# Kernel optimization log

Hardware: AMD Instinct MI355X
Metric: run time of the kernel (lower is better)

## Reference

```python
import jax, jax.numpy as jnp
import numpy as np

B, N, DIM, HEADS, DH, EDGE, DEPTH, K = 4, 128, 256, 8, 64, 64, 2, 512
INNER = HEADS * DH
SCALE = DH ** -0.5


def _ln(x, g, b, eps=1e-5):
    m = x.mean(-1, keepdims=True)
    v = ((x - m) ** 2).mean(-1, keepdims=True)
    return (x - m) / jnp.sqrt(v + eps) * g + b


def _rotate_half(x):
    # interleaved pairs: (d r) with r=2 -> (-x2, x1)
    xp = x.reshape(x.shape[:-1] + (-1, 2))
    x1, x2 = xp[..., 0], xp[..., 1]
    return jnp.stack((-x2, x1), axis=-1).reshape(x.shape)


def _gated_res(x, res, gw):
    gate = jax.nn.sigmoid(jnp.concatenate((x, res, x - res), axis=-1) @ gw)
    return x * gate + res * (1 - gate)


def forward(nodes, edges, edge_ln_g, edge_ln_b, ln1_g, ln1_b, w_exp, b_exp,
            w_q, b_q, w_kv, b_kv, w_ekv, b_ekv, w_out, b_out, gate1_w,
            ln2_g, ln2_b, w_ff1, b_ff1, w_ff2, b_ff2, gate2_w, codebook):
    b, n = nodes.shape[:2]
    # LayerNorm edges over channel dim: (B,C,N,N) -> (B,N,N,C)
    e = _ln(jnp.transpose(edges, (0, 2, 3, 1)), edge_ln_g, edge_ln_b)
    # rotary frequencies over positions, repeated pairwise -> (1, N, DH)
    inv = 1.0 / (10000.0 ** (jnp.arange(0, DH, 2, dtype=jnp.float32) / DH))
    fr = jnp.repeat(jnp.arange(n, dtype=jnp.float32)[:, None] * inv[None, :], 2, axis=-1)
    cos, sin = jnp.cos(fr)[None], jnp.sin(fr)[None]

    def heads3(t):  # (B,N,H*D) -> (B*H,N,D)
        return t.reshape(b, n, HEADS, DH).transpose(0, 2, 1, 3).reshape(b * HEADS, n, DH)

    for i in range(DEPTH):
        # PreNorm + edge-conditioned attention
        x = _ln(nodes, ln1_g[i], ln1_b[i])
        x = x @ w_exp[i] + b_exp[i]
        q = x @ w_q[i] + b_q[i]
        k, v = jnp.split(x @ w_kv[i] + b_kv[i], 2, axis=-1)
        ekv = e @ w_ekv[i] + b_ekv[i]  # (B,N,N,INNER)
        q, k, v = heads3(q), heads3(k), heads3(v)
        ekv = ekv.reshape(b, n, n, HEADS, DH).transpose(0, 3, 1, 2, 4).reshape(b * HEADS, n, n, DH)
        q = q * cos + _rotate_half(q) * sin
        k = k * cos + _rotate_half(k) * sin
        kk = k[:, None, :, :] + ekv  # (BH, i, j, d)
        vv = v[:, None, :, :] + ekv
        sim = jnp.einsum('bid,bijd->bij', q, kk) * SCALE
        att = jax.nn.softmax(sim, axis=-1)
        out = jnp.einsum('bij,bijd->bid', att, vv)
        out = out.reshape(b, HEADS, n, DH).transpose(0, 2, 1, 3).reshape(b, n, INNER)
        out = out @ w_out[i] + b_out[i]
        nodes = _gated_res(out, nodes, gate1_w[i])
        # PreNorm + FeedForward
        h = _ln(nodes, ln2_g[i], ln2_b[i])
        h = jax.nn.gelu(h @ w_ff1[i] + b_ff1[i], approximate=False) @ w_ff2[i] + b_ff2[i]
        nodes = _gated_res(h, nodes, gate2_w[i])

    # VQ codebook nearest-neighbor lookup with straight-through estimator
    z = nodes.reshape(-1, DIM)
    d = (z * z).sum(-1, keepdims=True) - 2.0 * z @ codebook.T + (codebook * codebook).sum(-1)[None, :]
    idx = jnp.argmin(d, axis=-1)
    zq = codebook[idx].reshape(b, n, DIM)
    return nodes + jax.lax.stop_gradient(zq - nodes)


def setup_inputs() -> dict:
    key = jax.random.key(0)
    ks = jax.random.split(key, 16)
    s = 0.02
    inp = {
        'nodes': jax.random.normal(ks[0], (B, N, DIM), jnp.float32),
        'edges': jax.random.normal(ks[1], (B, EDGE, N, N), jnp.float32),
        'edge_ln_g': jnp.ones((EDGE,), jnp.float32),
        'edge_ln_b': jnp.zeros((EDGE,), jnp.float32),
        'ln1_g': jnp.ones((DEPTH, DIM), jnp.float32),
        'ln1_b': jnp.zeros((DEPTH, DIM), jnp.float32),
        'w_exp': s * jax.random.normal(ks[2], (DEPTH, DIM, INNER), jnp.float32),
        'b_exp': jnp.zeros((DEPTH, INNER), jnp.float32),
        'w_q': s * jax.random.normal(ks[3], (DEPTH, INNER, INNER), jnp.float32),
        'b_q': jnp.zeros((DEPTH, INNER), jnp.float32),
        'w_kv': s * jax.random.normal(ks[4], (DEPTH, INNER, 2 * INNER), jnp.float32),
        'b_kv': jnp.zeros((DEPTH, 2 * INNER), jnp.float32),
        'w_ekv': s * jax.random.normal(ks[5], (DEPTH, EDGE, INNER), jnp.float32),
        'b_ekv': jnp.zeros((DEPTH, INNER), jnp.float32),
        'w_out': s * jax.random.normal(ks[6], (DEPTH, INNER, DIM), jnp.float32),
        'b_out': jnp.zeros((DEPTH, DIM), jnp.float32),
        'gate1_w': s * jax.random.normal(ks[7], (DEPTH, 3 * DIM, 1), jnp.float32),
        'ln2_g': jnp.ones((DEPTH, DIM), jnp.float32),
        'ln2_b': jnp.zeros((DEPTH, DIM), jnp.float32),
        'w_ff1': s * jax.random.normal(ks[8], (DEPTH, DIM, 4 * DIM), jnp.float32),
        'b_ff1': jnp.zeros((DEPTH, 4 * DIM), jnp.float32),
        'w_ff2': s * jax.random.normal(ks[9], (DEPTH, 4 * DIM, DIM), jnp.float32),
        'b_ff2': jnp.zeros((DEPTH, DIM), jnp.float32),
        'gate2_w': s * jax.random.normal(ks[10], (DEPTH, 3 * DIM, 1), jnp.float32),
        'codebook': jax.random.uniform(ks[11], (K, DIM), jnp.float32, -1.0 / K, 1.0 / K),
    }
    return inp


def reference(nodes, edges, edge_ln_g, edge_ln_b, ln1_g, ln1_b, w_exp, b_exp,
              w_q, b_q, w_kv, b_kv, w_ekv, b_ekv, w_out, b_out, gate1_w,
              ln2_g, ln2_b, w_ff1, b_ff1, w_ff2, b_ff2, gate2_w, codebook):
    return forward(nodes, edges, edge_ln_g, edge_ln_b, ln1_g, ln1_b, w_exp, b_exp,
                   w_q, b_q, w_kv, b_kv, w_ekv, b_ekv, w_out, b_out, gate1_w,
                   ln2_g, ln2_b, w_ff1, b_ff1, w_ff2, b_ff2, gate2_w, codebook)
```

## Files before the change

kernel.cpp:

```cpp
#include <hip/hip_runtime.h>
#include <math.h>


#define DEV __device__ __forceinline__

constexpr int Bn = 4, Nn = 128, DIMn = 256, HEADSn = 8, DHn = 64, EDGEn = 64,
              DEPTHn = 2, Kn = 512, INNERn = 512;
constexpr int QKVW = 1536;
constexpr int PART = 131072;

DEV float wave_reduce_sum(float v) {
#pragma unroll
  for (int m = 32; m >= 1; m >>= 1) v += __shfl_xor(v, m);
  return v;
}

DEV float block_reduce_sum_256(float v, float* red) {
  v = wave_reduce_sum(v);
  int tid = threadIdx.x;
  if ((tid & 63) == 0) red[tid >> 6] = v;
  __syncthreads();
  v = red[0] + red[1] + red[2] + red[3];
  __syncthreads();
  return v;
}

DEV float gelu_exact(float x) {
  return 0.5f * x * (1.f + erff(x * 0.70710678118654752f));
}

__global__ __launch_bounds__(256) void prep_kernel(
    const float* __restrict__ edges, const float* __restrict__ eg,
    const float* __restrict__ eb, float* __restrict__ e,
    float* __restrict__ eT, float* __restrict__ cost, float* __restrict__ sint,
    const float* __restrict__ nodes_in, const float* __restrict__ ln1_g,
    const float* __restrict__ ln1_b, float* __restrict__ xln,
    float* __restrict__ nodes, const float* __restrict__ wek,
    const float* __restrict__ w_out, const float* __restrict__ bek,
    const float* __restrict__ b_out, float* __restrict__ W2,
    float* __restrict__ b_out2, const float* __restrict__ w_exp,
    const float* __restrict__ b_exp, const float* __restrict__ w_q,
    const float* __restrict__ b_q, const float* __restrict__ w_kv,
    const float* __restrict__ b_kv, float* __restrict__ WqkvF,
    float* __restrict__ bqkvF) {
  __shared__ __align__(16) float smem[4480];
  int blk = blockIdx.x;
  int tid = threadIdx.x;

  if (blk < 12) {
    int t = blk;
    int l = t / 6, seg = t % 6;
    int n = seg * 256 + tid;
    const float* W;
    int ldw;
    float acc;
    if (n < 512) {
      W = w_q + (size_t)l * 512 * 512 + n;
      ldw = 512;
      acc = b_q[l * 512 + n];
    } else {
      W = w_kv + (size_t)l * 512 * 1024 + (n - 512);
      ldw = 1024;
      acc = b_kv[l * 1024 + (n - 512)];
    }
    const float* be = b_exp + l * 512;
#pragma unroll 8
    for (int k = 0; k < 512; ++k) acc += be[k] * W[(size_t)k * ldw];
    bqkvF[l * 1536 + n] = acc;
  } else if (blk < 396) {
    int t = blk - 12;
    int l = t / 192, r = t % 192;
    int by = r / 24, bx = r % 24;
    float* As = smem;
    float* Bs = smem + 32 * 34;
    int n0 = bx * 64;
    const float* Aab = w_exp + (size_t)l * 256 * 512 + (size_t)(by * 32) * 512;
    const float* Wb;
    int ldw;
    if (n0 < 512) {
      Wb = w_q + (size_t)l * 512 * 512 + n0;
      ldw = 512;
    } else {
      Wb = w_kv + (size_t)l * 512 * 1024 + (n0 - 512);
      ldw = 1024;
    }
    int arow = tid >> 3, acol = (tid & 7) << 2;
    int brow = tid >> 4, bcol = (tid & 15) << 2;
    int tx = tid & 15, ty = tid >> 4;
    float4 a_nxt = *(const float4*)(Aab + (size_t)arow * 512 + acol);
    float4 b0_nxt = *(const float4*)(Wb + (size_t)brow * ldw + bcol);
    float4 b1_nxt = *(const float4*)(Wb + (size_t)(brow + 16) * ldw + bcol);
    float acc[2][4] = {};
    for (int k0 = 0; k0 < 512; k0 += 32) {
      As[(acol + 0) * 34 + arow] = a_nxt.x;
      As[(acol + 1) * 34 + arow] = a_nxt.y;
      As[(acol + 2) * 34 + arow] = a_nxt.z;
      As[(acol + 3) * 34 + arow] = a_nxt.w;
      *(float4*)&Bs[brow * 68 + bcol] = b0_nxt;
      *(float4*)&Bs[(brow + 16) * 68 + bcol] = b1_nxt;
      __syncthreads();
      int kn = k0 + 32;
      if (kn < 512) {
        a_nxt = *(const float4*)(Aab + (size_t)arow * 512 + kn + acol);
        b0_nxt = *(const float4*)(Wb + (size_t)(kn + brow) * ldw + bcol);
        b1_nxt = *(const float4*)(Wb + (size_t)(kn + brow + 16) * ldw + bcol);
      }
#pragma unroll
      for (int kk = 0; kk < 32; ++kk) {
        float2 av = *(const float2*)&As[kk * 34 + ty * 2];
        float4 bv = *(const float4*)&Bs[kk * 68 + tx * 4];
        acc[0][0] += av.x * bv.x;
        acc[0][1] += av.x * bv.y;
        acc[0][2] += av.x * bv.z;
        acc[0][3] += av.x * bv.w;
        acc[1][0] += av.y * bv.x;
        acc[1][1] += av.y * bv.y;
        acc[1][2] += av.y * bv.z;
        acc[1][3] += av.y * bv.w;
      }
      __syncthreads();
    }
#pragma unroll
    for (int u = 0; u < 2; ++u) {
      int d = by * 32 + ty * 2 + u;
      float4 o = {acc[u][0], acc[u][1], acc[u][2], acc[u][3]};
      *(float4*)(WqkvF + (size_t)l * 256 * 1536 + (size_t)d * 1536 + n0 +
                 tx * 4) = o;
    }
  } else if (blk < 908) {
    float* ets = smem;
    int eidx = blk - 396;
    int i = eidx & 127, b = eidx >> 7;
    int j = tid & 127;
    bool act = tid < 128;
    float vals[EDGEn];
    float m = 0.f, inv = 0.f;
    if (act) {
      const float* src = edges + (size_t)b * EDGEn * Nn * Nn + i * Nn + j;
      float s = 0.f;
#pragma unroll
      for (int c = 0; c < EDGEn; ++c) {
        float x = src[(size_t)c * (Nn * Nn)];
        vals[c] = x;
        s += x;
      }
      m = s * (1.0f / 64.0f);
      float s2 = 0.f;
#pragma unroll
      for (int c = 0; c < EDGEn; ++c) {
        float d = vals[c] - m;
        s2 += d * d;
      }
      inv = 1.f / sqrtf(s2 * (1.0f / 64.0f) + 1e-5f);
    }
    float* dst = e + ((size_t)(b * Nn + i) * EDGEn) * Nn + j;
    float* dstT = eT + ((size_t)(b * Nn + i) * Nn) * EDGEn;
#pragma unroll
    for (int ch = 0; ch < 2; ++ch) {
      if (act) {
#pragma unroll
        for (int cc = 0; cc < 32; ++cc) {
          int c = ch * 32 + cc;
          float o = (vals[c] - m) * inv * eg[c] + eb[c];
          dst[(size_t)c * Nn] = o;
          ets[j * 33 + cc] = o;
        }
      }
      __syncthreads();
      if (act) {
#pragma unroll
        for (int it = 0; it < 8; ++it) {
          int f4 = it * 128 + j;
          int jj = f4 >> 3, c4 = (f4 & 7) << 2;
          float4 o4 = {ets[jj * 33 + c4], ets[jj * 33 + c4 + 1],
                       ets[jj * 33 + c4 + 2], ets[jj * 33 + c4 + 3]};
          *(float4*)(dstT + (size_t)jj * EDGEn + ch * 32 + c4) = o4;
        }
      }
      __syncthreads();
    }
  } else if (blk < 972) {
    int t = blk - 908;
    int l = t >> 5, h = (t >> 2) & 7, nt = t & 3;
    float* As = smem;
    float* Bs = smem + 64 * 36;
    const float* wekl = wek + (size_t)l * 64 * 512 + h * 64;
    const float* woutl =
        w_out + (size_t)l * 512 * 256 + (size_t)(h * 64) * 256 + nt * 64;
    int tx = tid & 15, ty = tid >> 4;
    float acc[4][4] = {};
    for (int d0 = 0; d0 < 64; d0 += 32) {
      for (int f = tid; f < 512; f += 256) {
        int c = f >> 3, d4 = (f & 7) << 2;
        *(float4*)&As[c * 36 + d4] =
            *(const float4*)(wekl + (size_t)c * 512 + d0 + d4);
      }
      for (int f = tid; f < 512; f += 256) {
        int dd = f >> 4, n4 = (f & 15) << 2;
        *(float4*)&Bs[dd * 68 + n4] =
            *(const float4*)(woutl + (size_t)(d0 + dd) * 256 + n4);
      }
      __syncthreads();
#pragma unroll
      for (int dd = 0; dd < 32; ++dd) {
        float4 bv = *(const float4*)&Bs[dd * 68 + tx * 4];
#pragma unroll
        for (int u = 0; u < 4; ++u) {
          float a = As[(ty * 4 + u) * 36 + dd];
          acc[u][0] += a * bv.x;
          acc[u][1] += a * bv.y;
          acc[u][2] += a * bv.z;
          acc[u][3] += a * bv.w;
        }
      }
      __syncthreads();
    }
#pragma unroll
    for (int u = 0; u < 4; ++u) {
      float4 o = {acc[u][0], acc[u][1], acc[u][2], acc[u][3]};
      *(float4*)(W2 + (size_t)l * 512 * 256 +
                 (size_t)(h * 64 + ty * 4 + u) * 256 + nt * 64 + tx * 4) = o;
    }
  } else if (blk < 980) {
    int t = blk - 972;
    int l = t >> 2, nt = t & 3;
    float* part = smem;
    int nn = tid & 63, kq = tid >> 6;
    const float* wcol = w_out + (size_t)l * 512 * 256 + nt * 64 + nn;
    float acc = 0.f;
    for (int k = kq * 128; k < kq * 128 + 128; ++k)
      acc += bek[l * 512 + k] * wcol[(size_t)k * 256];
    part[tid] = acc;
    __syncthreads();
    if (tid < 64)
      b_out2[l * 256 + nt * 64 + nn] =
          b_out[l * 256 + nt * 64 + nn] + part[nn] + part[64 + nn] +
          part[128 + nn] + part[192 + nn];
  } else if (blk < 996) {
    int t = (blk - 980) * 256 + tid;
    if (t < Nn * 32) {
      int n = t >> 5, p = t & 31;
      float inv = powf(10000.f, -(float)(2 * p) / 64.f);
      float fr = (float)n * inv;
      cost[t] = cosf(fr);
      sint[t] = sinf(fr);
    }
  } else {
    float* red = smem;
    int row = blk - 996;
    float v = nodes_in[(size_t)row * DIMn + tid];
    nodes[(size_t)row * DIMn + tid] = v;
    float m = block_reduce_sum_256(v, red) * (1.0f / 256.0f);
    float d = v - m;
    float var = block_reduce_sum_256(d * d, red) * (1.0f / 256.0f);
    float inv = 1.f / sqrtf(var + 1e-5f);
    xln[(size_t)row * DIMn + tid] = d * inv * ln1_g[tid] + ln1_b[tid];
  }
}

__global__ __launch_bounds__(256) void gemm_kernel(
    const float* __restrict__ A, const float* __restrict__ A2, int aact,
    const float* __restrict__ W1, int N1, const float* __restrict__ b1,
    const float* __restrict__ W2n, int N2, const float* __restrict__ b2,
    const float* __restrict__ Wkb, int Ksplit, float* __restrict__ C, int M,
    int Ntot, int K, int kspan, int act, const float* __restrict__ cost,
    const float* __restrict__ sint, float* __restrict__ kT) {
  __shared__ float As[32][34];
  __shared__ __align__(16) float Bs[32][68];
  int tid = threadIdx.x;
  int bx = blockIdx.x, by = blockIdx.y, zid = blockIdx.z;
  int tx = tid & 15, ty = tid >> 4;
  int arow = tid >> 3, acol = (tid & 7) << 2;
  int brow = tid >> 4, bcol = (tid & 15) << 2;
  int col0 = bx * 64;
  const float* W = W1;
  const float* bias = b1;
  int Nw = N1, wcol = col0;
  if (W2n && col0 >= N1) {
    W = W2n;
    bias = b2;
    Nw = N2;
    wcol = col0 - N1;
  }
  int kb = zid * kspan, kend = kb + kspan;
  const float* arp = A + (size_t)(by * 32 + arow) * K;
  const float* arp2 = A2 ? A2 + (size_t)(by * 32 + arow) * K : nullptr;

  auto load_a = [&](int kpos) -> float4 {
    float4 a = *(const float4*)(arp + kpos + acol);
    if (arp2) {
      float4 a2 = *(const float4*)(arp2 + kpos + acol);
      a.x += a2.x;
      a.y += a2.y;
      a.z += a2.z;
      a.w += a2.w;
    }
    if (aact == 1) {
      a.x = gelu_exact(a.x);
      a.y = gelu_exact(a.y);
      a.z = gelu_exact(a.z);
      a.w = gelu_exact(a.w);
    }
    return a;
  };

  float4 a_nxt = load_a(kb);
  const float* w0p;
  const float* w1p;
  {
    int kr0 = kb + brow, kr1 = kb + brow + 16;
    w0p = (Ksplit && kr0 >= Ksplit)
              ? Wkb + (size_t)(kr0 - Ksplit) * Nw + wcol + bcol
              : W + (size_t)kr0 * Nw + wcol + bcol;
    w1p = (Ksplit && kr1 >= Ksplit)
              ? Wkb + (size_t)(kr1 - Ksplit) * Nw + wcol + bcol
              : W + (size_t)kr1 * Nw + wcol + bcol;
  }
  float4 b0_nxt = *(const float4*)w0p;
  float4 b1_nxt = *(const float4*)w1p;

  float acc[2][4] = {};
  for (int k0 = kb; k0 < kend; k0 += 32) {
    As[acol + 0][arow] = a_nxt.x;
    As[acol + 1][arow] = a_nxt.y;
    As[acol + 2][arow] = a_nxt.z;
    As[acol + 3][arow] = a_nxt.w;
    *(float4*)&Bs[brow][bcol] = b0_nxt;
    *(float4*)&Bs[brow + 16][bcol] = b1_nxt;
    __syncthreads();
    int kn = k0 + 32;
    if (kn < kend) {
      a_nxt = load_a(kn);
      int kr0 = kn + brow, kr1 = kn + brow + 16;
      w0p = (Ksplit && kr0 >= Ksplit)
                ? Wkb + (size_t)(kr0 - Ksplit) * Nw + wcol + bcol
                : W + (size_t)kr0 * Nw + wcol + bcol;
      w1p = (Ksplit && kr1 >= Ksplit)
                ? Wkb + (size_t)(kr1 - Ksplit) * Nw + wcol + bcol
                : W + (size_t)kr1 * Nw + wcol + bcol;
      b0_nxt = *(const float4*)w0p;
      b1_nxt = *(const float4*)w1p;
    }
#pragma unroll
    for (int kk = 0; kk < 32; ++kk) {
      float2 av = *(const float2*)&As[kk][ty * 2];
      float4 bv = *(const float4*)&Bs[kk][tx * 4];
      acc[0][0] += av.x * bv.x;
      acc[0][1] += av.x * bv.y;
      acc[0][2] += av.x * bv.z;
      acc[0][3] += av.x * bv.w;
      acc[1][0] += av.y * bv.x;
      acc[1][1] += av.y * bv.y;
      acc[1][2] += av.y * bv.z;
      acc[1][3] += av.y * bv.w;
    }
    __syncthreads();
  }
  int ccol = wcol + tx * 4;
  bool ksec = (act == 4) && (col0 >= 512) && (col0 < 1024);
  float* trans = (float*)Bs;
  float* Cz = C + (size_t)zid * M * Ntot;
#pragma unroll
  for (int u = 0; u < 2; ++u) {
    int r = by * 32 + ty * 2 + u;
    float o[4];
#pragma unroll
    for (int w = 0; w < 4; ++w)
      o[w] = acc[u][w] + (zid == 0 ? bias[ccol + w] : 0.f);
    if (act == 1) {
#pragma unroll
      for (int w = 0; w < 4; ++w) o[w] = gelu_exact(o[w]);
    } else if (act == 4 && col0 < 1024) {
      int n = r & 127;
      int p0 = (ccol & 63) >> 1;
      float c0 = cost[n * 32 + p0], s0 = sint[n * 32 + p0];
      float c1 = cost[n * 32 + p0 + 1], s1 = sint[n * 32 + p0 + 1];
      float x0 = o[0], x1 = o[1], x2 = o[2], x3 = o[3];
      o[0] = x0 * c0 - x1 * s0;
      o[1] = x1 * c0 + x0 * s0;
      o[2] = x2 * c1 - x3 * s1;
      o[3] = x3 * c1 + x2 * s1;
    }
    if (ksec) {
#pragma unroll
      for (int w = 0; w < 4; ++w) trans[(tx * 4 + w) * 33 + ty * 2 + u] = o[w];
    } else {
      float4 o4 = {o[0], o[1], o[2], o[3]};
      *(float4*)(Cz + (size_t)r * Ntot + col0 + tx * 4) = o4;
    }
  }
  if (ksec) {
    __syncthreads();
    int h = (col0 - 512) >> 6;
    int bb = (by * 32) >> 7;
#pragma unroll
    for (int q = 0; q < 2; ++q) {
      int f4 = tid * 2 + q;
      int dl = f4 >> 3, j4 = (f4 & 7) << 2;
      int jj = (by * 32 + j4) & 127;
      float4 o4 = {trans[dl * 33 + j4], trans[dl * 33 + j4 + 1],
                   trans[dl * 33 + j4 + 2], trans[dl * 33 + j4 + 3]};
      *(float4*)(kT + ((size_t)(bb * 8 + h) * 64 + dl) * 128 + jj) = o4;
    }
  }
}

__global__ __launch_bounds__(128) void attn_kernel(
    const float* __restrict__ qkv, const float* __restrict__ e,
    const float* __restrict__ eT, const float* __restrict__ kT,
    const float* __restrict__ wek, const float* __restrict__ w_out,
    const float* __restrict__ W2, float* __restrict__ proj) {
  __shared__ __align__(16) float qs[256];
  __shared__ __align__(16) float qes[256];
  __shared__ __align__(16) float att[512];
  __shared__ float avh[512];
  __shared__ float aeh[512];
  __shared__ float wekh[64 * 65];
  int blk = blockIdx.x;
  int iq = blk & 31;
  int bh = blk >> 5;
  int h = bh & 7, b = bh >> 3;
  int i0 = iq * 4;
  int row0 = b * 128 + i0;
  int tid = threadIdx.x;

  for (int f = tid; f < 256; f += 128) {
    int ii = f >> 6, d = f & 63;
    qs[f] = qkv[(size_t)(row0 + ii) * QKVW + h * 64 + d];
  }
  for (int f = tid; f < 4096; f += 128) {
    int c = f >> 6, d = f & 63;
    wekh[c * 65 + d] = wek[(size_t)c * INNERn + h * 64 + d];
  }
  __syncthreads();

  for (int f = tid; f < 256; f += 128) {
    int ii = f >> 6, c = f & 63;
    float acc = 0.f;
#pragma unroll
    for (int d = 0; d < 64; ++d) acc += qs[ii * 64 + d] * wekh[c * 65 + d];
    qes[f] = acc;
  }
  __syncthreads();

  int i2 = tid >> 5, j4 = tid & 31;
  float s0 = 0.f, s1 = 0.f, s2 = 0.f, s3 = 0.f;
  {
    const float* ktb = kT + ((size_t)bh * 64) * 128 + j4 * 4;
#pragma unroll
    for (int d4 = 0; d4 < 64; d4 += 4) {
      float4 q4 = *(const float4*)&qs[i2 * 64 + d4];
      float4 k0 = *(const float4*)(ktb + (size_t)(d4 + 0) * 128);
      float4 k1 = *(const float4*)(ktb + (size_t)(d4 + 1) * 128);
      float4 k2 = *(const float4*)(ktb + (size_t)(d4 + 2) * 128);
      float4 k3 = *(const float4*)(ktb + (size_t)(d4 + 3) * 128);
      s0 += q4.x * k0.x + q4.y * k1.x + q4.z * k2.x + q4.w * k3.x;
      s1 += q4.x * k0.y + q4.y * k1.y + q4.z * k2.y + q4.w * k3.y;
      s2 += q4.x * k0.z + q4.y * k1.z + q4.z * k2.z + q4.w * k3.z;
      s3 += q4.x * k0.w + q4.y * k1.w + q4.z * k2.w + q4.w * k3.w;
    }
    const float* eb = e + ((size_t)(row0 + i2) * 64) * 128 + j4 * 4;
#pragma unroll
    for (int c4 = 0; c4 < 64; c4 += 4) {
      float4 qe4 = *(const float4*)&qes[i2 * 64 + c4];
      float4 e0 = *(const float4*)(eb + (size_t)(c4 + 0) * 128);
      float4 e1 = *(const float4*)(eb + (size_t)(c4 + 1) * 128);
      float4 e2 = *(const float4*)(eb + (size_t)(c4 + 2) * 128);
      float4 e3 = *(const float4*)(eb + (size_t)(c4 + 3) * 128);
      s0 += qe4.x * e0.x + qe4.y * e1.x + qe4.z * e2.x + qe4.w * e3.x;
      s1 += qe4.x * e0.y + qe4.y * e1.y + qe4.z * e2.y + qe4.w * e3.y;
      s2 += qe4.x * e0.z + qe4.y * e1.z + qe4.z * e2.z + qe4.w * e3.z;
      s3 += qe4.x * e0.w + qe4.y * e1.w + qe4.z * e2.w + qe4.w * e3.w;
    }
    s0 *= 0.125f;
    s1 *= 0.125f;
    s2 *= 0.125f;
    s3 *= 0.125f;
  }
  {
    float mx = fmaxf(fmaxf(s0, s1), fmaxf(s2, s3));
#pragma unroll
    for (int m = 16; m >= 1; m >>= 1) mx = fmaxf(mx, __shfl_xor(mx, m));
    float p0 = expf(s0 - mx), p1 = expf(s1 - mx), p2 = expf(s2 - mx),
          p3 = expf(s3 - mx);
    float sm = p0 + p1 + p2 + p3;
#pragma unroll
    for (int m = 16; m >= 1; m >>= 1) sm += __shfl_xor(sm, m);
    float inv = 1.f / sm;
    float4 a4 = {p0 * inv, p1 * inv, p2 * inv, p3 * inv};
    *(float4*)&att[i2 * 128 + j4 * 4] = a4;
  }
  __syncthreads();

  {
    int d = tid & 63, half = tid >> 6;
    float av0 = 0.f, av1 = 0.f, av2 = 0.f, av3 = 0.f;
    float ae0 = 0.f, ae1 = 0.f, ae2 = 0.f, ae3 = 0.f;
    const float* vb = qkv + (size_t)(b * 128) * QKVW + 1024 + h * 64 + d;
    const float* etb = eT + ((size_t)row0 * 128) * 64 + d;
    for (int jq = 0; jq < 16; ++jq) {
      int jb = half * 64 + jq * 4;
      float4 a0 = *(const float4*)&att[0 * 128 + jb];
      float4 a1 = *(const float4*)&att[1 * 128 + jb];
      float4 a2 = *(const float4*)&att[2 * 128 + jb];
      float4 a3 = *(const float4*)&att[3 * 128 + jb];
#pragma unroll
      for (int t = 0; t < 4; ++t) {
        int j = jb + t;
        float vv = vb[(size_t)j * QKVW];
        float at0 = ((const float*)&a0)[t];
        float at1 = ((const float*)&a1)[t];
        float at2 = ((const float*)&a2)[t];
        float at3 = ((const float*)&a3)[t];
        av0 += at0 * vv;
        av1 += at1 * vv;
        av2 += at2 * vv;
        av3 += at3 * vv;
        float e0 = etb[(size_t)j * 64];
        float e1 = etb[8192 + (size_t)j * 64];
        float e2 = etb[16384 + (size_t)j * 64];
        float e3 = etb[24576 + (size_t)j * 64];
        ae0 += at0 * e0;
        ae1 += at1 * e1;
        ae2 += at2 * e2;
        ae3 += at3 * e3;
      }
    }
    avh[half * 256 + 0 * 64 + d] = av0;
    avh[half * 256 + 1 * 64 + d] = av1;
    avh[half * 256 + 2 * 64 + d] = av2;
    avh[half * 256 + 3 * 64 + d] = av3;
    aeh[half * 256 + 0 * 64 + d] = ae0;
    aeh[half * 256 + 1 * 64 + d] = ae1;
    aeh[half * 256 + 2 * 64 + d] = ae2;
    aeh[half * 256 + 3 * 64 + d] = ae3;
  }
  __syncthreads();

  for (int f = tid; f < 256; f += 128) {
    int ii = f >> 6, dd = f & 63;
    att[ii * 128 + dd] = avh[ii * 64 + dd] + avh[256 + ii * 64 + dd];
    att[ii * 128 + 64 + dd] = aeh[ii * 64 + dd] + aeh[256 + ii * 64 + dd];
  }
  __syncthreads();

  {
    int rp = tid >> 6, n4 = (tid & 63) << 2;
    int r0 = rp * 2, r1 = rp * 2 + 1;
    float o0[4] = {}, o1[4] = {};
    const float* wo = w_out + (size_t)(h * 64) * 256 + n4;
#pragma unroll 8
    for (int k = 0; k < 64; ++k) {
      float4 w4 = *(const float4*)(wo + (size_t)k * 256);
      float a0 = att[r0 * 128 + k];
      float a1 = att[r1 * 128 + k];
      o0[0] += a0 * w4.x;
      o0[1] += a0 * w4.y;
      o0[2] += a0 * w4.z;
      o0[3] += a0 * w4.w;
      o1[0] += a1 * w4.x;
      o1[1] += a1 * w4.y;
      o1[2] += a1 * w4.z;
      o1[3] += a1 * w4.w;
    }
    const float* w2 = W2 + (size_t)(h * 64) * 256 + n4;
#pragma unroll 8
    for (int k = 0; k < 64; ++k) {
      float4 w4 = *(const float4*)(w2 + (size_t)k * 256);
      float a0 = att[r0 * 128 + 64 + k];
      float a1 = att[r1 * 128 + 64 + k];
      o0[0] += a0 * w4.x;
      o0[1] += a0 * w4.y;
      o0[2] += a0 * w4.z;
      o0[3] += a0 * w4.w;
      o1[0] += a1 * w4.x;
      o1[1] += a1 * w4.y;
      o1[2] += a1 * w4.z;
      o1[3] += a1 * w4.w;
    }
    float* pp = proj + (size_t)h * PART;
    float4 v0 = {o0[0], o0[1], o0[2], o0[3]};
    float4 v1 = {o1[0], o1[1], o1[2], o1[3]};
    *(float4*)(pp + (size_t)(row0 + r0) * 256 + n4) = v0;
    *(float4*)(pp + (size_t)(row0 + r1) * 256 + n4) = v1;
  }
}

__global__ __launch_bounds__(256) void gate_ln_kernel(
    const float* __restrict__ x, int nparts, const float* __restrict__ badd,
    float* __restrict__ nodes, const float* __restrict__ gw,
    const float* __restrict__ lng, const float* __restrict__ lnb,
    float* __restrict__ xln) {
  __shared__ float red[4];
  int row = blockIdx.x, tid = threadIdx.x;
  size_t off = (size_t)row * DIMn + tid;
  float xv = x[off];
  for (int p = 1; p < nparts; ++p) xv += x[off + (size_t)p * PART];
  if (badd) xv += badd[tid];
  float rv = nodes[off];
  float pv =
      xv * gw[tid] + rv * gw[DIMn + tid] + (xv - rv) * gw[2 * DIMn + tid];
  float ssum = block_reduce_sum_256(pv, red);
  float gsig = 1.f / (1.f + expf(-ssum));
  float nv = xv * gsig + rv * (1.f - gsig);
  nodes[off] = nv;
  if (lng) {
    float m = block_reduce_sum_256(nv, red) * (1.0f / 256.0f);
    float d = nv - m;
    float var = block_reduce_sum_256(d * d, red) * (1.0f / 256.0f);
    float inv = 1.f / sqrtf(var + 1e-5f);
    xln[off] = d * inv * lng[tid] + lnb[tid];
  }
}

__global__ __launch_bounds__(256) void vq_kernel(
    const float* __restrict__ nodes, const float* __restrict__ codebook,
    float* __restrict__ out) {
  __shared__ __align__(16) float zs[4 * 256];
  __shared__ float wval[4][4];
  __shared__ int widx[4][4];
  __shared__ int fidx[4];
  int row0 = blockIdx.x * 4;
  int tid = threadIdx.x;
  for (int f = tid; f < 1024; f += 256) zs[f] = nodes[(size_t)row0 * DIMn + f];
  __syncthreads();
  int k1 = tid, k2 = tid + 256;
  const float4* c1p = (const float4*)(codebook + (size_t)k1 * DIMn);
  const float4* c2p = (const float4*)(codebook + (size_t)k2 * DIMn);
  float dot[4][2] = {};
  float cc0 = 0.f, cc1 = 0.f;
#pragma unroll 8
  for (int d4 = 0; d4 < 64; ++d4) {
    float4 c1 = c1p[d4], c2 = c2p[d4];
    cc0 += c1.x * c1.x + c1.y * c1.y + c1.z * c1.z + c1.w * c1.w;
    cc1 += c2.x * c2.x + c2.y * c2.y + c2.z * c2.z + c2.w * c2.w;
#pragma unroll
    for (int r = 0; r < 4; ++r) {
      float4 z = *(const float4*)&zs[r * 256 + d4 * 4];
      dot[r][0] += c1.x * z.x + c1.y * z.y + c1.z * z.z + c1.w * z.w;
      dot[r][1] += c2.x * z.x + c2.y * z.y + c2.z * z.z + c2.w * z.w;
    }
  }
  int lane = tid & 63, w = tid >> 6;
#pragma unroll
  for (int r = 0; r < 4; ++r) {
    float bv = cc0 - 2.f * dot[r][0];
    int bi = k1;
    float v2 = cc1 - 2.f * dot[r][1];
    if (v2 < bv) {
      bv = v2;
      bi = k2;
    }
#pragma unroll
    for (int m = 32; m >= 1; m >>= 1) {
      float ov = __shfl_xor(bv, m);
      int oi = __shfl_xor(bi, m);
      if (ov < bv || (ov == bv && oi < bi)) {
        bv = ov;
        bi = oi;
      }
    }
    if (lane == 0) {
      wval[r][w] = bv;
      widx[r][w] = bi;
    }
  }
  __syncthreads();
  if (tid < 4) {
    float bb = wval[tid][0];
    int bi = widx[tid][0];
    for (int t = 1; t < 4; ++t)
      if (wval[tid][t] < bb || (wval[tid][t] == bb && widx[tid][t] < bi)) {
        bb = wval[tid][t];
        bi = widx[tid][t];
      }
    fidx[tid] = bi;
  }
  __syncthreads();
  for (int f = tid; f < 1024; f += 256) {
    int r = f >> 8, d = f & 255;
    float zv = zs[f];
    float zq = codebook[(size_t)fidx[r] * DIMn + d];
    out[(size_t)(row0 + r) * DIMn + d] = zv + (zq - zv);
  }
}

extern "C" void kernel_launch(void* const* d_in, const int* in_sizes, int n_in,
                              void* d_out, int out_size, void* d_ws,
                              size_t ws_size, hipStream_t stream) {
  const float* nodes_in = (const float*)d_in[0];
  const float* edges = (const float*)d_in[1];
  const float* edge_ln_g = (const float*)d_in[2];
  const float* edge_ln_b = (const float*)d_in[3];
  const float* ln1_g = (const float*)d_in[4];
  const float* ln1_b = (const float*)d_in[5];
  const float* w_exp = (const float*)d_in[6];
  const float* b_exp = (const float*)d_in[7];
  const float* w_q = (const float*)d_in[8];
  const float* b_q = (const float*)d_in[9];
  const float* w_kv = (const float*)d_in[10];
  const float* b_kv = (const float*)d_in[11];
  const float* w_ekv = (const float*)d_in[12];
  const float* b_ekv = (const float*)d_in[13];
  const float* w_out = (const float*)d_in[14];
  const float* b_out = (const float*)d_in[15];
  const float* gate1_w = (const float*)d_in[16];
  const float* ln2_g = (const float*)d_in[17];
  const float* ln2_b = (const float*)d_in[18];
  const float* w_ff1 = (const float*)d_in[19];
  const float* b_ff1 = (const float*)d_in[20];
  const float* w_ff2 = (const float*)d_in[21];
  const float* b_ff2 = (const float*)d_in[22];
  const float* gate2_w = (const float*)d_in[23];
  const float* codebook = (const float*)d_in[24];

  float* ws = (float*)d_ws;
  float* e_buf = ws;
  float* eT_buf = e_buf + 4194304;
  float* cost = eT_buf + 4194304;
  float* sint = cost + 4096;
  float* nodes = sint + 4096;
  float* xln = nodes + 131072;
  float* qkvb = xln + 131072;
  float* kTb = qkvb + 786432;
  float* proj = kTb + 262144;
  float* ff1 = proj + 1048576;
  float* W2buf = ff1 + 1048576;
  float* bout2 = W2buf + 262144;
  float* WqkvF = bout2 + 512;
  float* bqkvF = WqkvF + 786432;

  prep_kernel<<<1508, 256, 0, stream>>>(
      edges, edge_ln_g, edge_ln_b, e_buf, eT_buf, cost, sint, nodes_in, ln1_g,
      ln1_b, xln, nodes, w_ekv, w_out, b_ekv, b_out, W2buf, bout2, w_exp,
      b_exp, w_q, b_q, w_kv, b_kv, WqkvF, bqkvF);

  for (int l = 0; l < DEPTHn; ++l) {
    gemm_kernel<<<dim3(24, 16, 1), 256, 0, stream>>>(
        xln, nullptr, 0, WqkvF + (size_t)l * 256 * 1536, 1536,
        bqkvF + l * 1536, nullptr, 0, nullptr, nullptr, 0, qkvb, 512, QKVW,
        256, 256, 4, cost, sint, kTb);
    attn_kernel<<<1024, 128, 0, stream>>>(qkvb, e_buf, eT_buf, kTb,
                                          w_ekv + l * 64 * 512,
                                          w_out + l * 512 * 256,
                                          W2buf + l * 512 * 256, proj);
    gate_ln_kernel<<<512, 256, 0, stream>>>(
        proj, 8, bout2 + l * 256, nodes, gate1_w + l * 768, ln2_g + l * 256,
        ln2_b + l * 256, xln);
    gemm_kernel<<<dim3(16, 16, 2), 256, 0, stream>>>(
        xln, nullptr, 0, w_ff1 + l * 256 * 1024, 1024, b_ff1 + l * 1024,
        nullptr, 0, nullptr, nullptr, 0, ff1, 512, 1024, 256, 128, 0, cost,
        sint, nullptr);
    gemm_kernel<<<dim3(4, 16, 4), 256, 0, stream>>>(
        ff1, ff1 + 524288, 1, w_ff2 + l * 1024 * 256, 256, b_ff2 + l * 256,
        nullptr, 0, nullptr, nullptr, 0, proj, 512, 256, 1024, 256, 0, cost,
        sint, nullptr);
    const float* nlng = (l + 1 < DEPTHn) ? ln1_g + (l + 1) * 256 : nullptr;
    const float* nlnb = (l + 1 < DEPTHn) ? ln1_b + (l + 1) * 256 : nullptr;
    gate_ln_kernel<<<512, 256, 0, stream>>>(proj, 4, nullptr, nodes,
                                            gate2_w + l * 768, nlng, nlnb,
                                            xln);
  }
  vq_kernel<<<128, 256, 0, stream>>>(nodes, codebook, (float*)d_out);
}
```

Baseline: 319.0 us.

## Move edge LayerNorm and weight folding into first QKV gemm launch

After: 331.8 us. 1.04x slower.

```diff
diff --git a/kernel.cpp b/kernel.cpp
--- a/kernel.cpp
+++ b/kernel.cpp
@@ -29,21 +29,140 @@
   return 0.5f * x * (1.f + erff(x * 0.70710678118654752f));
 }
 
+
+DEV void edge_ln_block(int eidx, const float* __restrict__ edges,
+                       const float* __restrict__ eg,
+                       const float* __restrict__ eb, float* __restrict__ e,
+                       float* __restrict__ eT, float* smem) {
+  float* ets = smem;
+  float* redS = smem + 4224;
+  float* redQ = smem + 4480;
+  int tid = threadIdx.x;
+  int i = eidx & 127, b = eidx >> 7;
+  int j = tid & 127, half = tid >> 7;
+  const float* src = edges + (size_t)b * EDGEn * Nn * Nn +
+                     (size_t)(half * 32) * (Nn * Nn) + i * Nn + j;
+  float vals[32];
+  float s = 0.f, q = 0.f;
+#pragma unroll
+  for (int cc = 0; cc < 32; ++cc) {
+    float x = src[(size_t)cc * (Nn * Nn)];
+    vals[cc] = x;
+    s += x;
+    q += x * x;
+  }
+  redS[tid] = s;
+  redQ[tid] = q;
+  __syncthreads();
+  float ts = redS[j] + redS[j + 128];
+  float tq = redQ[j] + redQ[j + 128];
+  float m = ts * (1.0f / 64.0f);
+  float var = tq * (1.0f / 64.0f) - m * m;
+  float inv = 1.f / sqrtf(var + 1e-5f);
+  float* dst = e + ((size_t)(b * Nn + i) * EDGEn) * Nn + j;
+#pragma unroll
+  for (int cc = 0; cc < 32; ++cc) {
+    int c = half * 32 + cc;
+    float o = (vals[cc] - m) * inv * eg[c] + eb[c];
+    vals[cc] = o;
+    dst[(size_t)c * Nn] = o;
+  }
+  float* dstT = eT + ((size_t)(b * Nn + i) * Nn) * EDGEn;
+#pragma unroll
+  for (int ch = 0; ch < 2; ++ch) {
+    __syncthreads();
+    if (half == ch) {
+#pragma unroll
+      for (int cc = 0; cc < 32; ++cc) ets[j * 33 + cc] = vals[cc];
+    }
+    __syncthreads();
+#pragma unroll
+    for (int it = 0; it < 4; ++it) {
+      int f4 = it * 256 + tid;
+      int jj = f4 >> 3, c4 = (f4 & 7) << 2;
+      float4 o4 = {ets[jj * 33 + c4], ets[jj * 33 + c4 + 1],
+                   ets[jj * 33 + c4 + 2], ets[jj * 33 + c4 + 3]};
+      *(float4*)(dstT + (size_t)jj * EDGEn + ch * 32 + c4) = o4;
+    }
+  }
+}
+
+DEV void w2_fold_block(int t, const float* __restrict__ wek,
+                       const float* __restrict__ w_out, float* __restrict__ W2,
+                       float* smem) {
+  int l = t >> 5, h = (t >> 2) & 7, nt = t & 3;
+  float* As = smem;
+  float* Bs = smem + 2304;
+  const float* wekl = wek + (size_t)l * 64 * 512 + h * 64;
+  const float* woutl =
+      w_out + (size_t)l * 512 * 256 + (size_t)(h * 64) * 256 + nt * 64;
+  int tid = threadIdx.x;
+  int tx = tid & 15, ty = tid >> 4;
+  float acc[4][4] = {};
+  for (int d0 = 0; d0 < 64; d0 += 32) {
+    for (int f = tid; f < 512; f += 256) {
+      int c = f >> 3, d4 = (f & 7) << 2;
+      *(float4*)&As[c * 36 + d4] =
+          *(const float4*)(wekl + (size_t)c * 512 + d0 + d4);
+    }
+    for (int f = tid; f < 512; f += 256) {
+      int dd = f >> 4, n4 = (f & 15) << 2;
+      *(float4*)&Bs[dd * 68 + n4] =
+          *(const float4*)(woutl + (size_t)(d0 + dd) * 256 + n4);
+    }
+    __syncthreads();
+#pragma unroll
+    for (int dd = 0; dd < 32; ++dd) {
+      float4 bv = *(const float4*)&Bs[dd * 68 + tx * 4];
+#pragma unroll
+      for (int u = 0; u < 4; ++u) {
+        float a = As[(ty * 4 + u) * 36 + dd];
+        acc[u][0] += a * bv.x;
+        acc[u][1] += a * bv.y;
+        acc[u][2] += a * bv.z;
+        acc[u][3] += a * bv.w;
+      }
+    }
+    __syncthreads();
+  }
+#pragma unroll
+  for (int u = 0; u < 4; ++u) {
+    float4 o = {acc[u][0], acc[u][1], acc[u][2], acc[u][3]};
+    *(float4*)(W2 + (size_t)l * 512 * 256 + (size_t)(h * 64 + ty * 4 + u) * 256 +
+               nt * 64 + tx * 4) = o;
+  }
+}
+
+DEV void bout2_block(int t, const float* __restrict__ w_out,
+                     const float* __restrict__ bek,
+                     const float* __restrict__ b_out,
+                     float* __restrict__ b_out2, float* smem) {
+  int l = t >> 2, nt = t & 3;
+  float* part = smem;
+  int tid = threadIdx.x;
+  int nn = tid & 63, kq = tid >> 6;
+  const float* wcol = w_out + (size_t)l * 512 * 256 + nt * 64 + nn;
+  float acc = 0.f;
+  for (int k = kq * 128; k < kq * 128 + 128; ++k)
+    acc += bek[l * 512 + k] * wcol[(size_t)k * 256];
+  part[tid] = acc;
+  __syncthreads();
+  if (tid < 64)
+    b_out2[l * 256 + nt * 64 + nn] =
+        b_out[l * 256 + nt * 64 + nn] + part[nn] + part[64 + nn] +
+        part[128 + nn] + part[192 + nn];
+}
+
 __global__ __launch_bounds__(256) void prep_kernel(
-    const float* __restrict__ edges, const float* __restrict__ eg,
-    const float* __restrict__ eb, float* __restrict__ e,
-    float* __restrict__ eT, float* __restrict__ cost, float* __restrict__ sint,
-    const float* __restrict__ nodes_in, const float* __restrict__ ln1_g,
-    const float* __restrict__ ln1_b, float* __restrict__ xln,
-    float* __restrict__ nodes, const float* __restrict__ wek,
-    const float* __restrict__ w_out, const float* __restrict__ bek,
-    const float* __restrict__ b_out, float* __restrict__ W2,
-    float* __restrict__ b_out2, const float* __restrict__ w_exp,
-    const float* __restrict__ b_exp, const float* __restrict__ w_q,
-    const float* __restrict__ b_q, const float* __restrict__ w_kv,
-    const float* __restrict__ b_kv, float* __restrict__ WqkvF,
-    float* __restrict__ bqkvF) {
-  __shared__ __align__(16) float smem[4480];
+    const float* __restrict__ cost_dummy, float* __restrict__ cost,
+    float* __restrict__ sint, const float* __restrict__ nodes_in,
+    const float* __restrict__ ln1_g, const float* __restrict__ ln1_b,
+    float* __restrict__ xln, float* __restrict__ nodes,
+    const float* __restrict__ w_exp, const float* __restrict__ b_exp,
+    const float* __restrict__ w_q, const float* __restrict__ b_q,
+    const float* __restrict__ w_kv, const float* __restrict__ b_kv,
+    float* __restrict__ WqkvF, float* __restrict__ bqkvF) {
+  __shared__ __align__(16) float smem[3264];
   int blk = blockIdx.x;
   int tid = threadIdx.x;
 
@@ -127,117 +246,8 @@
       *(float4*)(WqkvF + (size_t)l * 256 * 1536 + (size_t)d * 1536 + n0 +
                  tx * 4) = o;
     }
-  } else if (blk < 908) {
-    float* ets = smem;
-    int eidx = blk - 396;
-    int i = eidx & 127, b = eidx >> 7;
-    int j = tid & 127;
-    bool act = tid < 128;
-    float vals[EDGEn];
-    float m = 0.f, inv = 0.f;
-    if (act) {
-      const float* src = edges + (size_t)b * EDGEn * Nn * Nn + i * Nn + j;
-      float s = 0.f;
-#pragma unroll
-      for (int c = 0; c < EDGEn; ++c) {
-        float x = src[(size_t)c * (Nn * Nn)];
-        vals[c] = x;
-        s += x;
-      }
-      m = s * (1.0f / 64.0f);
-      float s2 = 0.f;
-#pragma unroll
-      for (int c = 0; c < EDGEn; ++c) {
-        float d = vals[c] - m;
-        s2 += d * d;
-      }
-      inv = 1.f / sqrtf(s2 * (1.0f / 64.0f) + 1e-5f);
-    }
-    float* dst = e + ((size_t)(b * Nn + i) * EDGEn) * Nn + j;
-    float* dstT = eT + ((size_t)(b * Nn + i) * Nn) * EDGEn;
-#pragma unroll
-    for (int ch = 0; ch < 2; ++ch) {
-      if (act) {
-#pragma unroll
-        for (int cc = 0; cc < 32; ++cc) {
-          int c = ch * 32 + cc;
-          float o = (vals[c] - m) * inv * eg[c] + eb[c];
-          dst[(size_t)c * Nn] = o;
-          ets[j * 33 + cc] = o;
-        }
-      }
-      __syncthreads();
-      if (act) {
-#pragma unroll
-        for (int it = 0; it < 8; ++it) {
-          int f4 = it * 128 + j;
-          int jj = f4 >> 3, c4 = (f4 & 7) << 2;
-          float4 o4 = {ets[jj * 33 + c4], ets[jj * 33 + c4 + 1],
-                       ets[jj * 33 + c4 + 2], ets[jj * 33 + c4 + 3]};
-          *(float4*)(dstT + (size_t)jj * EDGEn + ch * 32 + c4) = o4;
-        }
-      }
-      __syncthreads();
-    }
-  } else if (blk < 972) {
-    int t = blk - 908;
-    int l = t >> 5, h = (t >> 2) & 7, nt = t & 3;
-    float* As = smem;
-    float* Bs = smem + 64 * 36;
-    const float* wekl = wek + (size_t)l * 64 * 512 + h * 64;
-    const float* woutl =
-        w_out + (size_t)l * 512 * 256 + (size_t)(h * 64) * 256 + nt * 64;
-    int tx = tid & 15, ty = tid >> 4;
-    float acc[4][4] = {};
-    for (int d0 = 0; d0 < 64; d0 += 32) {
-      for (int f = tid; f < 512; f += 256) {
-        int c = f >> 3, d4 = (f & 7) << 2;
-        *(float4*)&As[c * 36 + d4] =
-            *(const float4*)(wekl + (size_t)c * 512 + d0 + d4);
-      }
-      for (int f = tid; f < 512; f += 256) {
-        int dd = f >> 4, n4 = (f & 15) << 2;
-        *(float4*)&Bs[dd * 68 + n4] =
-            *(const float4*)(woutl + (size_t)(d0 + dd) * 256 + n4);
-      }
-      __syncthreads();
-#pragma unroll
-      for (int dd = 0; dd < 32; ++dd) {
-        float4 bv = *(const float4*)&Bs[dd * 68 + tx * 4];
-#pragma unroll
-        for (int u = 0; u < 4; ++u) {
-          float a = As[(ty * 4 + u) * 36 + dd];
-          acc[u][0] += a * bv.x;
-          acc[u][1] += a * bv.y;
-          acc[u][2] += a * bv.z;
-          acc[u][3] += a * bv.w;
-        }
-      }
-      __syncthreads();
-    }
-#pragma unroll
-    for (int u = 0; u < 4; ++u) {
-      float4 o = {acc[u][0], acc[u][1], acc[u][2], acc[u][3]};
-      *(float4*)(W2 + (size_t)l * 512 * 256 +
-                 (size_t)(h * 64 + ty * 4 + u) * 256 + nt * 64 + tx * 4) = o;
-    }
-  } else if (blk < 980) {
-    int t = blk - 972;
-    int l = t >> 2, nt = t & 3;
-    float* part = smem;
-    int nn = tid & 63, kq = tid >> 6;
-    const float* wcol = w_out + (size_t)l * 512 * 256 + nt * 64 + nn;
-    float acc = 0.f;
-    for (int k = kq * 128; k < kq * 128 + 128; ++k)
-      acc += bek[l * 512 + k] * wcol[(size_t)k * 256];
-    part[tid] = acc;
-    __syncthreads();
-    if (tid < 64)
-      b_out2[l * 256 + nt * 64 + nn] =
-          b_out[l * 256 + nt * 64 + nn] + part[nn] + part[64 + nn] +
-          part[128 + nn] + part[192 + nn];
-  } else if (blk < 996) {
-    int t = (blk - 980) * 256 + tid;
+  } else if (blk < 412) {
+    int t = (blk - 396) * 256 + tid;
     if (t < Nn * 32) {
       int n = t >> 5, p = t & 31;
       float inv = powf(10000.f, -(float)(2 * p) / 64.f);
@@ -247,7 +257,7 @@
     }
   } else {
     float* red = smem;
-    int row = blk - 996;
+    int row = blk - 412;
     float v = nodes_in[(size_t)row * DIMn + tid];
     nodes[(size_t)row * DIMn + tid] = v;
     float m = block_reduce_sum_256(v, red) * (1.0f / 256.0f);
@@ -264,9 +274,26 @@
     const float* __restrict__ W2n, int N2, const float* __restrict__ b2,
     const float* __restrict__ Wkb, int Ksplit, float* __restrict__ C, int M,
     int Ntot, int K, int kspan, int act, const float* __restrict__ cost,
-    const float* __restrict__ sint, float* __restrict__ kT) {
-  __shared__ float As[32][34];
-  __shared__ __align__(16) float Bs[32][68];
+    const float* __restrict__ sint, float* __restrict__ kT,
+    const float* __restrict__ edges, const float* __restrict__ eg,
+    const float* __restrict__ ebv, float* __restrict__ e,
+    float* __restrict__ eT, const float* __restrict__ wek,
+    const float* __restrict__ w_out_g, const float* __restrict__ bek,
+    const float* __restrict__ b_out_g, float* __restrict__ W2,
+    float* __restrict__ b_out2) {
+  __shared__ __align__(16) float smem[4736];
+  if (blockIdx.y >= 16) {
+    int extra = (blockIdx.y - 16) * gridDim.x + blockIdx.x;
+    if (extra < 512)
+      edge_ln_block(extra, edges, eg, ebv, e, eT, smem);
+    else if (extra < 576)
+      w2_fold_block(extra - 512, wek, w_out_g, W2, smem);
+    else if (extra < 584)
+      bout2_block(extra - 576, w_out_g, bek, b_out_g, b_out2, smem);
+    return;
+  }
+  float* As = smem;
+  float* Bs = smem + 1088;
   int tid = threadIdx.x;
   int bx = blockIdx.x, by = blockIdx.y, zid = blockIdx.z;
   int tx = tid & 15, ty = tid >> 4;
@@ -321,12 +348,12 @@
 
   float acc[2][4] = {};
   for (int k0 = kb; k0 < kend; k0 += 32) {
-    As[acol + 0][arow] = a_nxt.x;
-    As[acol + 1][arow] = a_nxt.y;
-    As[acol + 2][arow] = a_nxt.z;
-    As[acol + 3][arow] = a_nxt.w;
-    *(float4*)&Bs[brow][bcol] = b0_nxt;
-    *(float4*)&Bs[brow + 16][bcol] = b1_nxt;
+    As[(acol + 0) * 34 + arow] = a_nxt.x;
+    As[(acol + 1) * 34 + arow] = a_nxt.y;
+    As[(acol + 2) * 34 + arow] = a_nxt.z;
+    As[(acol + 3) * 34 + arow] = a_nxt.w;
+    *(float4*)&Bs[brow * 68 + bcol] = b0_nxt;
+    *(float4*)&Bs[(brow + 16) * 68 + bcol] = b1_nxt;
     __syncthreads();
     int kn = k0 + 32;
     if (kn < kend) {
@@ -343,8 +370,8 @@
     }
 #pragma unroll
     for (int kk = 0; kk < 32; ++kk) {
-      float2 av = *(const float2*)&As[kk][ty * 2];
-      float4 bv = *(const float4*)&Bs[kk][tx * 4];
+      float2 av = *(const float2*)&As[kk * 34 + ty * 2];
+      float4 bv = *(const float4*)&Bs[kk * 68 + tx * 4];
       acc[0][0] += av.x * bv.x;
       acc[0][1] += av.x * bv.y;
       acc[0][2] += av.x * bv.z;
@@ -358,7 +385,7 @@
   }
   int ccol = wcol + tx * 4;
   bool ksec = (act == 4) && (col0 >= 512) && (col0 < 1024);
-  float* trans = (float*)Bs;
+  float* trans = Bs;
   float* Cz = C + (size_t)zid * M * Ntot;
 #pragma unroll
   for (int u = 0; u < 2; ++u) {
@@ -730,16 +757,17 @@
   float* WqkvF = bout2 + 512;
   float* bqkvF = WqkvF + 786432;
 
-  prep_kernel<<<1508, 256, 0, stream>>>(
-      edges, edge_ln_g, edge_ln_b, e_buf, eT_buf, cost, sint, nodes_in, ln1_g,
-      ln1_b, xln, nodes, w_ekv, w_out, b_ekv, b_out, W2buf, bout2, w_exp,
-      b_exp, w_q, b_q, w_kv, b_kv, WqkvF, bqkvF);
+  prep_kernel<<<924, 256, 0, stream>>>(nullptr, cost, sint, nodes_in, ln1_g,
+                                       ln1_b, xln, nodes, w_exp, b_exp, w_q,
+                                       b_q, w_kv, b_kv, WqkvF, bqkvF);
 
   for (int l = 0; l < DEPTHn; ++l) {
-    gemm_kernel<<<dim3(24, 16, 1), 256, 0, stream>>>(
+    dim3 qgrid = (l == 0) ? dim3(24, 41, 1) : dim3(24, 16, 1);
+    gemm_kernel<<<qgrid, 256, 0, stream>>>(
         xln, nullptr, 0, WqkvF + (size_t)l * 256 * 1536, 1536,
         bqkvF + l * 1536, nullptr, 0, nullptr, nullptr, 0, qkvb, 512, QKVW,
-        256, 256, 4, cost, sint, kTb);
+        256, 256, 4, cost, sint, kTb, edges, edge_ln_g, edge_ln_b, e_buf,
+        eT_buf, w_ekv, w_out, b_ekv, b_out, W2buf, bout2);
     attn_kernel<<<1024, 128, 0, stream>>>(qkvb, e_buf, eT_buf, kTb,
                                           w_ekv + l * 64 * 512,
                                           w_out + l * 512 * 256,
@@ -750,11 +778,13 @@
     gemm_kernel<<<dim3(16, 16, 2), 256, 0, stream>>>(
         xln, nullptr, 0, w_ff1 + l * 256 * 1024, 1024, b_ff1 + l * 1024,
         nullptr, 0, nullptr, nullptr, 0, ff1, 512, 1024, 256, 128, 0, cost,
-        sint, nullptr);
+        sint, nullptr, nullptr, nullptr, nullptr, nullptr, nullptr, nullptr,
+        nullptr, nullptr, nullptr, nullptr, nullptr);
     gemm_kernel<<<dim3(4, 16, 4), 256, 0, stream>>>(
         ff1, ff1 + 524288, 1, w_ff2 + l * 1024 * 256, 256, b_ff2 + l * 256,
         nullptr, 0, nullptr, nullptr, 0, proj, 512, 256, 1024, 256, 0, cost,
-        sint, nullptr);
+        sint, nullptr, nullptr, nullptr, nullptr, nullptr, nullptr, nullptr,
+        nullptr, nullptr, nullptr, nullptr, nullptr);
     const float* nlng = (l + 1 < DEPTHn) ? ln1_g + (l + 1) * 256 : nullptr;
     const float* nlnb = (l + 1 < DEPTHn) ? ln1_b + (l + 1) * 256 : nullptr;
     gate_ln_kernel<<<512, 256, 0, stream>>>(proj, 4, nullptr, nodes,
```
